# Kernel tuning notes

Hardware: AMD Instinct MI355X
Metric: run time of the kernel (lower is better)

Reference implementation:

```python
import jax, jax.numpy as jnp
import numpy as np

EPS = 1e-5

def conv1d(x, w, b, pad):
    # x: (B,Cin,T), w: (Cout,Cin,K)
    y = jax.lax.conv_general_dilated(x, w, (1,), [(pad, pad)],
                                     dimension_numbers=('NCW', 'OIW', 'NCW'))
    return y + b[None, :, None]

def group_norm(x, scale, bias, groups):
    B, C, T = x.shape
    xg = x.reshape(B, groups, C // groups, T)
    mu = xg.mean(axis=(2, 3), keepdims=True)
    var = xg.var(axis=(2, 3), keepdims=True)
    xn = ((xg - mu) * jax.lax.rsqrt(var + EPS)).reshape(B, C, T)
    return xn * scale[None, :, None] + bias[None, :, None]

def setup_inputs() -> dict:
    key = jax.random.key(0)
    ks = jax.random.split(key, 16)
    T, B = 1024, 128
    class_size, style_size, char_style_size = 80, 256, 64
    hidden, n_out = 128, 1
    cin = class_size + style_size + char_style_size  # 400
    def w(k, shape, fan_in):
        return jax.random.normal(k, shape, jnp.float32) * (1.0 / np.sqrt(fan_in))
    inp = {
        'input': jax.random.normal(ks[0], (T, B, class_size), jnp.float32),
        'g_style': jax.random.normal(ks[1], (B, style_size), jnp.float32),
        'spacing_style': jax.random.normal(ks[2], (B, 8), jnp.float32),
        'char_style': jax.random.normal(ks[3], (B, class_size, char_style_size), jnp.float32),
        'conv1_w': w(ks[4], (hidden, cin, 3), cin * 3),
        'conv1_b': jnp.zeros((hidden,), jnp.float32),
        'gn1_s': jnp.ones((hidden,), jnp.float32),
        'gn1_b': jnp.zeros((hidden,), jnp.float32),
        'conv2_w': w(ks[5], (hidden // 2, hidden, 3), hidden * 3),
        'conv2_b': jnp.zeros((hidden // 2,), jnp.float32),
        'gn2_s': jnp.ones((hidden // 2,), jnp.float32),
        'gn2_b': jnp.zeros((hidden // 2,), jnp.float32),
        'conv3_w': w(ks[6], (hidden // 4, hidden // 2, 3), (hidden // 2) * 3),
        'conv3_b': jnp.zeros((hidden // 4,), jnp.float32),
        'gn3_s': jnp.ones((hidden // 4,), jnp.float32),
        'gn3_b': jnp.zeros((hidden // 4,), jnp.float32),
        'conv4_w': w(ks[7], (n_out, hidden // 4, 1), hidden // 4),
        'conv4_b': jnp.zeros((n_out,), jnp.float32),
        'mean': jnp.full((1, n_out), 2.0, jnp.float32),
        'std': jnp.full((1, n_out), 1.0, jnp.float32),
    }
    return inp

def reference(input, g_style, spacing_style, char_style,
              conv1_w, conv1_b, gn1_s, gn1_b,
              conv2_w, conv2_b, gn2_s, gn2_b,
              conv3_w, conv3_b, gn3_s, gn3_b,
              conv4_w, conv4_b, mean, std):
    T, B, _ = input.shape
    # vectorized char-style gather (replaces the python double loop)
    text_chars = jnp.argmax(input, axis=2)                      # (T,B)
    input_style = char_style[jnp.arange(B)[None, :], text_chars]  # (T,B,Dc)
    gs = jnp.broadcast_to(g_style[None], (T,) + g_style.shape)    # (T,B,Ds)
    x = jnp.concatenate([input, gs, input_style], axis=2)         # (T,B,Cin)
    x = x.transpose(1, 2, 0)                                      # (B,Cin,T)
    x = jax.nn.relu(group_norm(conv1d(x, conv1_w, conv1_b, 1), gn1_s, gn1_b, 32))
    x = jax.nn.relu(group_norm(conv1d(x, conv2_w, conv2_b, 1), gn2_s, gn2_b, 32))
    x = jax.nn.relu(group_norm(conv1d(x, conv3_w, conv3_b, 1), gn3_s, gn3_b, 32))
    x = conv1d(x, conv4_w, conv4_b, 0)                            # (B,n_out,T)
    out = x.transpose(2, 0, 1)                                    # (T,B,n_out)
    return out * std + mean
```

## Files before the change

kernel.cpp:

```cpp
#include <hip/hip_runtime.h>
#include <hip/hip_bf16.h>

#define T_LEN 1024
#define BATCH 128
#define NM 131072

typedef __attribute__((ext_vector_type(8))) short short8;
typedef __attribute__((ext_vector_type(4))) float f32x4;
typedef __attribute__((ext_vector_type(4))) uint uint4e;

__device__ __forceinline__ float b2f(ushort u) {
  union { uint i; float f; } c; c.i = ((uint)u) << 16; return c.f;
}
__device__ __forceinline__ ushort f2b(float f) {
  __hip_bfloat16 h = __float2bfloat16(f);
  return *reinterpret_cast<ushort*>(&h);
}
__device__ __forceinline__ uint pack2(float a, float b) {
  return (uint)f2b(a) | ((uint)f2b(b) << 16);
}

__global__ __launch_bounds__(1024) void k_pre(const float* __restrict__ inp, const float* __restrict__ cs,
                                              ushort* __restrict__ X1) {
  __shared__ __align__(16) ushort L[8][32][160];
  int bid = blockIdx.x, tid = threadIdx.x;
  int b0 = (bid >> 5) * 8;
  int t0 = (bid & 31) * 32;
  int q = tid & 3;
  int u = tid >> 2;
  int bp = u & 7, tp = u >> 3;
  int b = b0 + bp, t = t0 + tp;
  int m = t*128 + b;
  const float* rp = inp + (size_t)m*80 + q*20;
  float v[20];
  #pragma unroll
  for (int i = 0; i < 5; ++i) {
    float4 u4 = *(const float4*)(rp + i*4);
    v[i*4+0]=u4.x; v[i*4+1]=u4.y; v[i*4+2]=u4.z; v[i*4+3]=u4.w;
  }
  float best = v[0]; int bi = q*20;
  #pragma unroll
  for (int i = 1; i < 20; ++i) if (v[i] > best) { best = v[i]; bi = q*20 + i; }
  #pragma unroll
  for (int d = 1; d <= 2; d <<= 1) {
    float ob = __shfl_xor(best, d);
    int   oi = __shfl_xor(bi, d);
    if (ob > best || (ob == best && oi < bi)) { best = ob; bi = oi; }
  }
  ushort* lr = &L[bp][tp][0];
  #pragma unroll
  for (int i = 0; i < 5; ++i) {
    uint2 pk; pk.x = pack2(v[i*4], v[i*4+1]); pk.y = pack2(v[i*4+2], v[i*4+3]);
    *(uint2*)(lr + q*20 + i*4) = pk;
  }
  *(uint2*)(lr + 80 + q*4) = make_uint2(0u, 0u);
  const float* crow = cs + ((size_t)b*80 + bi)*64 + q*16;
  #pragma unroll
  for (int i = 0; i < 4; ++i) {
    float4 u4 = *(const float4*)(crow + i*4);
    uint2 pk; pk.x = pack2(u4.x, u4.y); pk.y = pack2(u4.z, u4.w);
    *(uint2*)(lr + 96 + q*16 + i*4) = pk;
  }
  __syncthreads();
  int wave = tid >> 6, lane = tid & 63;
  int p = wave >> 1, h = wave & 1;
  ushort* dst = X1 + ((size_t)(b0 + p)*1024 + t0)*160 + h*2560;
  const ushort* src = &L[p][0][0] + h*2560;
  #pragma unroll
  for (int it = 0; it < 5; ++it) {
    int r = it*64 + lane;
    uint4e val = *(const uint4e*)(src + r*8);
    __builtin_nontemporal_store(val, (uint4e*)(dst + r*8));
  }
}

__global__ __launch_bounds__(256) void k_prep(const float* __restrict__ gsty,
    const float* __restrict__ w1, const float* __restrict__ b1,
    const float* __restrict__ w2, const float* __restrict__ w3,
    float* __restrict__ Gfull, float* __restrict__ Gk0, float* __restrict__ Gk2,
    ushort* __restrict__ Wp1, ushort* __restrict__ Wp2, ushort* __restrict__ Wp3) {
  int bid = blockIdx.x, tid = threadIdx.x;
  if (bid < 128) {
    int b = bid;
    __shared__ float gl[256];
    gl[tid] = gsty[b*256 + tid];
    __syncthreads();
    if (tid < 128) {
      int o = tid;
      const float* wr = w1 + (size_t)o*1200 + 240;
      float s0 = 0.f, s1 = 0.f, s2 = 0.f;
      for (int c = 0; c < 256; ++c) {
        float g = gl[c];
        s0 += wr[c*3+0]*g; s1 += wr[c*3+1]*g; s2 += wr[c*3+2]*g;
      }
      Gk0[b*128+o] = s0;
      Gk2[b*128+o] = s2;
      Gfull[b*128+o] = s0 + s1 + s2 + b1[o];
    }
  } else {
    int e = (bid - 128)*256 + tid;
    if (e < 61440) {
      int o = e / 480, r = e % 480, k = r / 160, c = r % 160;
      float v = 0.f;
      if (c < 80)       v = w1[(size_t)o*1200 + c*3 + k];
      else if (c >= 96) v = w1[(size_t)o*1200 + (336 + (c-96))*3 + k];
      Wp1[e] = f2b(v);
    } else if (e < 61440 + 24576) {
      int e2 = e - 61440;
      int o = e2/384, r = e2%384, k = r/128, c = r%128;
      Wp2[e2] = f2b(w2[(size_t)o*384 + c*3 + k]);
    } else if (e < 61440 + 24576 + 6144) {
      int e3 = e - 61440 - 24576;
      int o = e3/192, r = e3%192, k = r/64, c = r%64;
      Wp3[e3] = f2b(w3[(size_t)o*192 + c*3 + k]);
    }
  }
}

__device__ __forceinline__ uint4 c1_ldx(const ushort* X1b, int cc, int t0, int task) {
  int r = task >> 2, q = task & 3;
  int t = t0 - 1 + r;
  if (t >= 0 && t < T_LEN) return *(const uint4*)(X1b + (size_t)t*160 + cc*32 + q*8);
  return make_uint4(0u,0u,0u,0u);
}
__device__ __forceinline__ short8 c1_ldw(const ushort* Wp1, int cc, int task) {
  int o = task / 12, seg = task % 12;
  int k = seg >> 2, oct = seg & 3;
  return *(const short8*)(Wp1 + (size_t)o*480 + k*160 + cc*32 + oct*8);
}
__device__ __forceinline__ void c1_wrx(ushort (*Xsb)[40], int task, uint4 v) {
  int r = task >> 2, q = task & 3;
  *(uint4*)&Xsb[r][q*8] = v;
}
__device__ __forceinline__ void c1_wrw(ushort (*Wsb)[104], int task, short8 v) {
  int o = task / 12, seg = task % 12;
  *(short8*)&Wsb[o][seg*8] = v;
}

__global__ __launch_bounds__(256) void k_conv1(const ushort* __restrict__ X1, const ushort* __restrict__ Wp1,
    const float* __restrict__ Gfull, const float* __restrict__ Gk0, const float* __restrict__ Gk2,
    ushort* __restrict__ y1, float2* __restrict__ part1) {
  __shared__ __align__(16) ushort Xs[2][130][40];
  __shared__ __align__(16) ushort Ws[2][128][104];
  __shared__ float gf[128], g0v[128], g2v[128];
  __shared__ float ps[4][128], pq[4][128];
  int b = blockIdx.x, tt = blockIdx.y;
  int t0 = tt * 128;
  int tid = threadIdx.x, lane = tid & 63, wave = tid >> 6;
  int ln = lane & 15, lq = lane >> 4, wt = wave * 32;
  const ushort* X1b = X1 + (size_t)b * 163840;

  if (tid < 128) {
    gf[tid]  = Gfull[b*128 + tid];
    g0v[tid] = Gk0[b*128 + tid];
    g2v[tid] = Gk2[b*128 + tid];
  }
  f32x4 acc[2][8];
  #pragma unroll
  for (int m = 0; m < 2; ++m)
    #pragma unroll
    for (int n = 0; n < 8; ++n) { f32x4 z = {0.f,0.f,0.f,0.f}; acc[m][n] = z; }

  uint4 rx0, rx1, rx2;
  short8 rw[6];

  rx0 = c1_ldx(X1b, 0, t0, tid);
  rx1 = c1_ldx(X1b, 0, t0, tid + 256);
  if (tid < 8) rx2 = c1_ldx(X1b, 0, t0, tid + 512);
  #pragma unroll
  for (int i = 0; i < 6; ++i) rw[i] = c1_ldw(Wp1, 0, tid + i*256);
  c1_wrx(Xs[0], tid, rx0);
  c1_wrx(Xs[0], tid + 256, rx1);
  if (tid < 8) c1_wrx(Xs[0], tid + 512, rx2);
  #pragma unroll
  for (int i = 0; i < 6; ++i) c1_wrw(Ws[0], tid + i*256, rw[i]);
  __syncthreads();

  for (int cc = 0; cc < 5; ++cc) {
    bool more = (cc < 4);
    if (more) {
      rx0 = c1_ldx(X1b, cc+1, t0, tid);
      rx1 = c1_ldx(X1b, cc+1, t0, tid + 256);
      if (tid < 8) rx2 = c1_ldx(X1b, cc+1, t0, tid + 512);
      #pragma unroll
      for (int i = 0; i < 6; ++i) rw[i] = c1_ldw(Wp1, cc+1, tid + i*256);
    }
    int cur = cc & 1;
    #pragma unroll
    for (int k = 0; k < 3; ++k) {
      short8 a0 = *(const short8*)&Xs[cur][wt + ln + k][lq*8];
      short8 a1 = *(const short8*)&Xs[cur][wt + 16 + ln + k][lq*8];
      #pragma unroll
      for (int nt = 0; nt < 8; ++nt) {
        short8 bb = *(const short8*)&Ws[cur][nt*16 + ln][k*32 + lq*8];
        acc[0][nt] = __builtin_amdgcn_mfma_f32_16x16x32_bf16(a0, bb, acc[0][nt], 0, 0, 0);
        acc[1][nt] = __builtin_amdgcn_mfma_f32_16x16x32_bf16(a1, bb, acc[1][nt], 0, 0, 0);
      }
    }
    if (more) {
      int nxt = cur ^ 1;
      c1_wrx(Xs[nxt], tid, rx0);
      c1_wrx(Xs[nxt], tid + 256, rx1);
      if (tid < 8) c1_wrx(Xs[nxt], tid + 512, rx2);
      #pragma unroll
      for (int i = 0; i < 6; ++i) c1_wrw(Ws[nxt], tid + i*256, rw[i]);
    }
    __syncthreads();
  }

  #pragma unroll
  for (int nt = 0; nt < 8; ++nt) {
    int o = nt*16 + ln;
    float add = gf[o];
    float s = 0.f, sq = 0.f;
    #pragma unroll
    for (int mt = 0; mt < 2; ++mt) {
      int tb = t0 + wt + mt*16 + lq*4;
      float vv[4];
      #pragma unroll
      for (int r = 0; r < 4; ++r) {
        float v = acc[mt][nt][r] + add;
        int t = tb + r;
        if (t == 0) v -= g0v[o];
        if (t == T_LEN-1) v -= g2v[o];
        vv[r] = v; s += v; sq += v*v;
      }
      uint2 pk;
      pk.x = pack2(vv[0], vv[1]);
      pk.y = pack2(vv[2], vv[3]);
      *(uint2*)(y1 + ((size_t)b*128 + o)*T_LEN + tb) = pk;
    }
    s  += __shfl_xor(s, 16);  s  += __shfl_xor(s, 32);
    sq += __shfl_xor(sq, 16); sq += __shfl_xor(sq, 32);
    if (lane < 16) { ps[wave][o] = s; pq[wave][o] = sq; }
  }
  __syncthreads();
  if (tid < 128) {
    float S = ps[0][tid]+ps[1][tid]+ps[2][tid]+ps[3][tid];
    float Q = pq[0][tid]+pq[1][tid]+pq[2][tid]+pq[3][tid];
    part1[((size_t)b*128 + tid)*8 + tt] = make_float2(S, Q);
  }
}

__device__ __forceinline__ short8 mid_ldw(const ushort* Wp, int cin, int cc, int task) {
  int o = task / 12, seg = task % 12;
  int k = seg >> 2, oct = seg & 3;
  return *(const short8*)(Wp + ((size_t)o*3 + k)*cin + cc*32 + oct*8);
}
__device__ __forceinline__ void mid_wrw(ushort (*Wsb)[104], int task, short8 v) {
  int o = task / 12, seg = task % 12;
  *(short8*)&Wsb[o][seg*8] = v;
}

template<int NC, int CO, int NT, int CPG>
__global__ __launch_bounds__(256) void k_convmid(const ushort* __restrict__ xin,
    const ushort* __restrict__ Wp, const float* __restrict__ bias,
    const float2* __restrict__ partin, const float* __restrict__ gs, const float* __restrict__ gb,
    ushort* __restrict__ yout, float2* __restrict__ part) {
  constexpr int CIN = NC*32;
  constexpr int NG = CIN/CPG;
  __shared__ __align__(16) ushort Xs[2][130][40];
  __shared__ __align__(16) ushort Ws[2][CO][104];
  __shared__ float2 affl[CIN];
  __shared__ float ssb[CIN], qqb[CIN];
  __shared__ float2 gmr[NG];
  __shared__ float bl[CO];
  __shared__ float ps[4][CO], pq[4][CO];
  int b = blockIdx.x, tt = blockIdx.y, t0 = tt*128;
  int tid = threadIdx.x, lane = tid & 63, wave = tid >> 6;
  int ln = lane & 15, lq = lane >> 4, wt = wave*32;
  int cp = (tid & 15)*2, j = tid >> 4;
  int er = (tid < 32) ? 0 : 129, eci = tid & 31;
  const ushort* xb = xin + (size_t)b * CIN * T_LEN;

  if (tid < CIN) {
    const float2* p = partin + (size_t)(b*CIN + tid)*8;
    float S = 0.f, Q = 0.f;
    #pragma unroll
    for (int j2 = 0; j2 < 8; ++j2) { float2 v = p[j2]; S += v.x; Q += v.y; }
    ssb[tid] = S; qqb[tid] = Q;
  }
  if (tid < CO)  bl[tid]  = bias[tid];

  f32x4 acc[2][NT];
  #pragma unroll
  for (int m = 0; m < 2; ++m)
    #pragma unroll
    for (int n = 0; n < NT; ++n) { f32x4 z = {0.f,0.f,0.f,0.f}; acc[m][n] = z; }

  short8 v0, v1;
  ushort ev = 0;
  short8 rw0, rw1, rw2;
  int te = t0 - 1 + er;

  {
    const ushort* s0 = xb + (size_t)cp * T_LEN + t0 + j*8;
    v0 = *(const short8*)s0;
    v1 = *(const short8*)(s0 + T_LEN);
    ev = 0;
    if (tid < 64 && te >= 0 && te < T_LEN) ev = xb[(size_t)eci * T_LEN + te];
    rw0 = mid_ldw(Wp, CIN, 0, tid);
    if constexpr (CO == 64) {
      rw1 = mid_ldw(Wp, CIN, 0, tid + 256);
      rw2 = mid_ldw(Wp, CIN, 0, tid + 512);
    } else {
      if (tid < 128) rw1 = mid_ldw(Wp, CIN, 0, tid + 256);
    }
  }
  __syncthreads();
  if (tid < NG) {
    float S = 0.f, Q = 0.f;
    #pragma unroll
    for (int ci = 0; ci < CPG; ++ci) { S += ssb[tid*CPG+ci]; Q += qqb[tid*CPG+ci]; }
    float invn = 1.f / (float)(CPG * T_LEN);
    float m = S * invn;
    float var = Q * invn - m*m;
    gmr[tid] = make_float2(m, rsqrtf(var + 1e-5f));
  }
  __syncthreads();
  if (tid < CIN) {
    float2 mr = gmr[tid / CPG];
    float a = mr.y * gs[tid];
    affl[tid] = make_float2(a, gb[tid] - mr.x * a);
  }
  __syncthreads();
  {
    float2 A0 = affl[cp], A1 = affl[cp+1];
    #pragma unroll
    for (int e = 0; e < 8; ++e) {
      float f0 = fmaxf(0.f, b2f((ushort)v0[e])*A0.x + A0.y);
      float f1 = fmaxf(0.f, b2f((ushort)v1[e])*A1.x + A1.y);
      *(uint*)&Xs[0][1 + j*8 + e][cp] = pack2(f0, f1);
    }
    if (tid < 64) {
      ushort val = 0;
      if (te >= 0 && te < T_LEN) { float2 A = affl[eci]; val = f2b(fmaxf(0.f, b2f(ev)*A.x + A.y)); }
      Xs[0][er][eci] = val;
    }
    mid_wrw(Ws[0], tid, rw0);
    if constexpr (CO == 64) {
      mid_wrw(Ws[0], tid + 256, rw1);
      mid_wrw(Ws[0], tid + 512, rw2);
    } else {
      if (tid < 128) mid_wrw(Ws[0], tid + 256, rw1);
    }
  }
  __syncthreads();

  for (int cc = 0; cc < NC; ++cc) {
    bool more = (cc + 1 < NC);
    if (more) {
      const ushort* s0 = xb + (size_t)((cc+1)*32 + cp) * T_LEN + t0 + j*8;
      v0 = *(const short8*)s0;
      v1 = *(const short8*)(s0 + T_LEN);
      ev = 0;
      if (tid < 64 && te >= 0 && te < T_LEN) ev = xb[(size_t)((cc+1)*32 + eci) * T_LEN + te];
      rw0 = mid_ldw(Wp, CIN, cc+1, tid);
      if constexpr (CO == 64) {
        rw1 = mid_ldw(Wp, CIN, cc+1, tid + 256);
        rw2 = mid_ldw(Wp, CIN, cc+1, tid + 512);
      } else {
        if (tid < 128) rw1 = mid_ldw(Wp, CIN, cc+1, tid + 256);
      }
    }
    int cur = cc & 1;
    #pragma unroll
    for (int k = 0; k < 3; ++k) {
      short8 a0 = *(const short8*)&Xs[cur][wt + ln + k][lq*8];
      short8 a1 = *(const short8*)&Xs[cur][wt + 16 + ln + k][lq*8];
      #pragma unroll
      for (int nt = 0; nt < NT; ++nt) {
        short8 bb = *(const short8*)&Ws[cur][nt*16 + ln][k*32 + lq*8];
        acc[0][nt] = __builtin_amdgcn_mfma_f32_16x16x32_bf16(a0, bb, acc[0][nt], 0, 0, 0);
        acc[1][nt] = __builtin_amdgcn_mfma_f32_16x16x32_bf16(a1, bb, acc[1][nt], 0, 0, 0);
      }
    }
    if (more) {
      int nxt = cur ^ 1;
      float2 A0 = affl[(cc+1)*32 + cp], A1 = affl[(cc+1)*32 + cp + 1];
      #pragma unroll
      for (int e = 0; e < 8; ++e) {
        float f0 = fmaxf(0.f, b2f((ushort)v0[e])*A0.x + A0.y);
        float f1 = fmaxf(0.f, b2f((ushort)v1[e])*A1.x + A1.y);
        *(uint*)&Xs[nxt][1 + j*8 + e][cp] = pack2(f0, f1);
      }
      if (tid < 64) {
        ushort val = 0;
        if (te >= 0 && te < T_LEN) { float2 A = affl[(cc+1)*32 + eci]; val = f2b(fmaxf(0.f, b2f(ev)*A.x + A.y)); }
        Xs[nxt][er][eci] = val;
      }
      mid_wrw(Ws[nxt], tid, rw0);
      if constexpr (CO == 64) {
        mid_wrw(Ws[nxt], tid + 256, rw1);
        mid_wrw(Ws[nxt], tid + 512, rw2);
      } else {
        if (tid < 128) mid_wrw(Ws[nxt], tid + 256, rw1);
      }
    }
    __syncthreads();
  }

  #pragma unroll
  for (int nt = 0; nt < NT; ++nt) {
    int o = nt*16 + ln;
    float add = bl[o];
    float s = 0.f, sq = 0.f;
    #pragma unroll
    for (int mt = 0; mt < 2; ++mt) {
      int tb = t0 + wt + mt*16 + lq*4;
      float vv[4];
      #pragma unroll
      for (int r = 0; r < 4; ++r) {
        float v = acc[mt][nt][r] + add;
        vv[r] = v; s += v; sq += v*v;
      }
      uint2 pk;
      pk.x = pack2(vv[0], vv[1]);
      pk.y = pack2(vv[2], vv[3]);
      *(uint2*)(yout + ((size_t)b*CO + o)*T_LEN + tb) = pk;
    }
    s  += __shfl_xor(s, 16);  s  += __shfl_xor(s, 32);
    sq += __shfl_xor(sq, 16); sq += __shfl_xor(sq, 32);
    if (lane < 16) { ps[wave][o] = s; pq[wave][o] = sq; }
  }
  __syncthreads();
  if (tid < CO) {
    float S = ps[0][tid]+ps[1][tid]+ps[2][tid]+ps[3][tid];
    float Q = pq[0][tid]+pq[1][tid]+pq[2][tid]+pq[3][tid];
    part[((size_t)b*CO + tid)*8 + tt] = make_float2(S, Q);
  }
}

__global__ __launch_bounds__(256) void k_final(const ushort* __restrict__ y3, const float2* __restrict__ part3,
    const float* __restrict__ s3, const float* __restrict__ b3,
    const float* __restrict__ w4, const float* __restrict__ b4,
    const float* __restrict__ mn, const float* __restrict__ sd, float* __restrict__ out) {
  int b = blockIdx.x;
  int t = blockIdx.y * 256 + threadIdx.x;
  __shared__ float wl[32];
  __shared__ float2 al[32];
  if (threadIdx.x < 32) {
    int c = threadIdx.x;
    const float2* p = part3 + (size_t)(b*32 + c)*8;
    float S = 0.f, Q = 0.f;
    #pragma unroll
    for (int j = 0; j < 8; ++j) { float2 v = p[j]; S += v.x; Q += v.y; }
    float invn = 1.f / (float)T_LEN;
    float m = S * invn;
    float var = Q * invn - m*m;
    float rs = rsqrtf(var + 1e-5f);
    float a = rs * s3[c];
    al[c] = make_float2(a, b3[c] - m*a);
    wl[c] = w4[c];
  }
  __syncthreads();
  float s = b4[0];
  #pragma unroll 8
  for (int c = 0; c < 32; ++c) {
    float v = b2f(y3[((size_t)b*32 + c)*T_LEN + t]);
    float2 A = al[c];
    s += wl[c] * fmaxf(0.f, v*A.x + A.y);
  }
  out[(size_t)t*BATCH + b] = s*sd[0] + mn[0];
}

extern "C" void kernel_launch(void* const* d_in, const int* in_sizes, int n_in,
                              void* d_out, int out_size, void* d_ws, size_t ws_size,
                              hipStream_t stream) {
  const float* inp  = (const float*)d_in[0];
  const float* gsty = (const float*)d_in[1];
  const float* cs   = (const float*)d_in[3];
  const float* w1   = (const float*)d_in[4];
  const float* b1   = (const float*)d_in[5];
  const float* gn1s = (const float*)d_in[6];
  const float* gn1b = (const float*)d_in[7];
  const float* w2   = (const float*)d_in[8];
  const float* b2   = (const float*)d_in[9];
  const float* gn2s = (const float*)d_in[10];
  const float* gn2b = (const float*)d_in[11];
  const float* w3   = (const float*)d_in[12];
  const float* b3   = (const float*)d_in[13];
  const float* gn3s = (const float*)d_in[14];
  const float* gn3b = (const float*)d_in[15];
  const float* w4   = (const float*)d_in[16];
  const float* b4   = (const float*)d_in[17];
  const float* mn   = (const float*)d_in[18];
  const float* sd   = (const float*)d_in[19];
  float* out = (float*)d_out;
  ushort* wsu = (ushort*)d_ws;

  ushort* X1  = wsu;
  ushort* Wp1 = X1 + (size_t)20971520;
  ushort* Wp2 = Wp1 + 61440;
  ushort* Wp3 = Wp2 + 24576;
  float* Gfull = (float*)(Wp3 + 6144);
  float* Gk0   = Gfull + 16384;
  float* Gk2   = Gk0 + 16384;
  ushort* y1 = (ushort*)(Gk2 + 16384);
  ushort* y2 = y1 + (size_t)NM*128;
  ushort* y3 = y2 + (size_t)NM*64;
  float2* part1 = (float2*)(y3 + (size_t)NM*32);
  float2* part2 = part1 + 131072;
  float2* part3 = part2 + 65536;

  k_pre<<<512, 1024, 0, stream>>>(inp, cs, X1);
  k_prep<<<488, 256, 0, stream>>>(gsty, w1, b1, w2, w3,
                                  Gfull, Gk0, Gk2, Wp1, Wp2, Wp3);
  k_conv1<<<dim3(128,8), 256, 0, stream>>>(X1, Wp1, Gfull, Gk0, Gk2, y1, part1);
  k_convmid<4,64,4,4><<<dim3(128,8), 256, 0, stream>>>(y1, Wp2, b2, part1, gn1s, gn1b, y2, part2);
  k_convmid<2,32,2,2><<<dim3(128,8), 256, 0, stream>>>(y2, Wp3, b3, part2, gn2s, gn2b, y3, part3);
  k_final<<<dim3(128,4), 256, 0, stream>>>(y3, part3, gn3s, gn3b, w4, b4, mn, sd, out);
}
```

Before: 101.7 us.

## Gather char-style rows inside conv1 instead of materializing padded input tensor

The preprocessing kernel now writes only the bf16 one-hot input in its native (T,B,80) layout plus an argmax index per position, rather than a transposed, padded 160-channel tensor that also holds the gathered char-style rows. Conv1 reads the class channels directly from that layout and gathers the char-style rows from the fp32 source table using the indices staged in shared memory, converting to bf16 on the fly. This cuts the intermediate write and read traffic roughly in half. The cost is strided per-row loads in conv1 (80-element rows spaced by batch) and scattered fp32 gathers, which may coalesce less well.

```diff
diff --git a/kernel.cpp b/kernel.cpp
--- a/kernel.cpp
+++ b/kernel.cpp
@@ -7,7 +7,6 @@
 
 typedef __attribute__((ext_vector_type(8))) short short8;
 typedef __attribute__((ext_vector_type(4))) float f32x4;
-typedef __attribute__((ext_vector_type(4))) uint uint4e;
 
 __device__ __forceinline__ float b2f(ushort u) {
   union { uint i; float f; } c; c.i = ((uint)u) << 16; return c.f;
@@ -20,18 +19,12 @@
   return (uint)f2b(a) | ((uint)f2b(b) << 16);
 }
 
-__global__ __launch_bounds__(1024) void k_pre(const float* __restrict__ inp, const float* __restrict__ cs,
-                                              ushort* __restrict__ X1) {
-  __shared__ __align__(16) ushort L[8][32][160];
-  int bid = blockIdx.x, tid = threadIdx.x;
-  int b0 = (bid >> 5) * 8;
-  int t0 = (bid & 31) * 32;
+__global__ __launch_bounds__(256) void k_pre(const float* __restrict__ inp,
+                                             ushort* __restrict__ Xm, int* __restrict__ idx) {
+  int tid = threadIdx.x;
+  int m = blockIdx.x * 64 + (tid >> 2);
   int q = tid & 3;
-  int u = tid >> 2;
-  int bp = u & 7, tp = u >> 3;
-  int b = b0 + bp, t = t0 + tp;
-  int m = t*128 + b;
-  const float* rp = inp + (size_t)m*80 + q*20;
+  const float* rp = inp + (size_t)m * 80 + q * 20;
   float v[20];
   #pragma unroll
   for (int i = 0; i < 5; ++i) {
@@ -47,30 +40,12 @@
     int   oi = __shfl_xor(bi, d);
     if (ob > best || (ob == best && oi < bi)) { best = ob; bi = oi; }
   }
-  ushort* lr = &L[bp][tp][0];
+  if (q == 0) idx[m] = bi;
+  ushort* orow = Xm + (size_t)m * 80 + q * 20;
   #pragma unroll
   for (int i = 0; i < 5; ++i) {
     uint2 pk; pk.x = pack2(v[i*4], v[i*4+1]); pk.y = pack2(v[i*4+2], v[i*4+3]);
-    *(uint2*)(lr + q*20 + i*4) = pk;
-  }
-  *(uint2*)(lr + 80 + q*4) = make_uint2(0u, 0u);
-  const float* crow = cs + ((size_t)b*80 + bi)*64 + q*16;
-  #pragma unroll
-  for (int i = 0; i < 4; ++i) {
-    float4 u4 = *(const float4*)(crow + i*4);
-    uint2 pk; pk.x = pack2(u4.x, u4.y); pk.y = pack2(u4.z, u4.w);
-    *(uint2*)(lr + 96 + q*16 + i*4) = pk;
-  }
-  __syncthreads();
-  int wave = tid >> 6, lane = tid & 63;
-  int p = wave >> 1, h = wave & 1;
-  ushort* dst = X1 + ((size_t)(b0 + p)*1024 + t0)*160 + h*2560;
-  const ushort* src = &L[p][0][0] + h*2560;
-  #pragma unroll
-  for (int it = 0; it < 5; ++it) {
-    int r = it*64 + lane;
-    uint4e val = *(const uint4e*)(src + r*8);
-    __builtin_nontemporal_store(val, (uint4e*)(dst + r*8));
+    *(uint2*)(orow + i*4) = pk;
   }
 }
 
@@ -117,10 +92,31 @@
   }
 }
 
-__device__ __forceinline__ uint4 c1_ldx(const ushort* X1b, int cc, int t0, int task) {
+__device__ __forceinline__ uint4 c1_ldx16(const ushort* __restrict__ Xm, int b, int cc, int t0, int task) {
   int r = task >> 2, q = task & 3;
   int t = t0 - 1 + r;
-  if (t >= 0 && t < T_LEN) return *(const uint4*)(X1b + (size_t)t*160 + cc*32 + q*8);
+  int c8 = cc*32 + q*8;
+  if (t >= 0 && t < T_LEN && c8 < 80)
+    return *(const uint4*)(Xm + ((size_t)t*BATCH + b)*80 + c8);
+  return make_uint4(0u,0u,0u,0u);
+}
+__device__ __forceinline__ uint4 packf(float4 a, float4 b) {
+  uint4 p;
+  p.x = pack2(a.x, a.y); p.y = pack2(a.z, a.w);
+  p.z = pack2(b.x, b.y); p.w = pack2(b.z, b.w);
+  return p;
+}
+__device__ __forceinline__ uint4 c1_ldcs(const float* __restrict__ cs, const int* idxs,
+                                         int b, int cc, int t0, int task) {
+  int r = task >> 2, q = task & 3;
+  int t = t0 - 1 + r;
+  if (t >= 0 && t < T_LEN) {
+    int jc = idxs[r];
+    const float* src = cs + ((size_t)b*80 + jc)*64 + (cc-3)*32 + q*8;
+    float4 fa = *(const float4*)src;
+    float4 fb = *(const float4*)(src + 4);
+    return packf(fa, fb);
+  }
   return make_uint4(0u,0u,0u,0u);
 }
 __device__ __forceinline__ short8 c1_ldw(const ushort* Wp1, int cc, int task) {
@@ -137,19 +133,24 @@
   *(short8*)&Wsb[o][seg*8] = v;
 }
 
-__global__ __launch_bounds__(256) void k_conv1(const ushort* __restrict__ X1, const ushort* __restrict__ Wp1,
+__global__ __launch_bounds__(256) void k_conv1(const ushort* __restrict__ Xm, const float* __restrict__ cs,
+    const int* __restrict__ idx, const ushort* __restrict__ Wp1,
     const float* __restrict__ Gfull, const float* __restrict__ Gk0, const float* __restrict__ Gk2,
     ushort* __restrict__ y1, float2* __restrict__ part1) {
   __shared__ __align__(16) ushort Xs[2][130][40];
   __shared__ __align__(16) ushort Ws[2][128][104];
   __shared__ float gf[128], g0v[128], g2v[128];
   __shared__ float ps[4][128], pq[4][128];
+  __shared__ int idxs[130];
   int b = blockIdx.x, tt = blockIdx.y;
   int t0 = tt * 128;
   int tid = threadIdx.x, lane = tid & 63, wave = tid >> 6;
   int ln = lane & 15, lq = lane >> 4, wt = wave * 32;
-  const ushort* X1b = X1 + (size_t)b * 163840;
-
+
+  if (tid < 130) {
+    int t = t0 - 1 + tid;
+    idxs[tid] = (t >= 0 && t < T_LEN) ? idx[t*BATCH + b] : 0;
+  }
   if (tid < 128) {
     gf[tid]  = Gfull[b*128 + tid];
     g0v[tid] = Gk0[b*128 + tid];
@@ -164,9 +165,9 @@
   uint4 rx0, rx1, rx2;
   short8 rw[6];
 
-  rx0 = c1_ldx(X1b, 0, t0, tid);
-  rx1 = c1_ldx(X1b, 0, t0, tid + 256);
-  if (tid < 8) rx2 = c1_ldx(X1b, 0, t0, tid + 512);
+  rx0 = c1_ldx16(Xm, b, 0, t0, tid);
+  rx1 = c1_ldx16(Xm, b, 0, t0, tid + 256);
+  if (tid < 8) rx2 = c1_ldx16(Xm, b, 0, t0, tid + 512);
   #pragma unroll
   for (int i = 0; i < 6; ++i) rw[i] = c1_ldw(Wp1, 0, tid + i*256);
   c1_wrx(Xs[0], tid, rx0);
@@ -179,9 +180,15 @@
   for (int cc = 0; cc < 5; ++cc) {
     bool more = (cc < 4);
     if (more) {
-      rx0 = c1_ldx(X1b, cc+1, t0, tid);
-      rx1 = c1_ldx(X1b, cc+1, t0, tid + 256);
-      if (tid < 8) rx2 = c1_ldx(X1b, cc+1, t0, tid + 512);
+      if (cc + 1 < 3) {
+        rx0 = c1_ldx16(Xm, b, cc+1, t0, tid);
+        rx1 = c1_ldx16(Xm, b, cc+1, t0, tid + 256);
+        if (tid < 8) rx2 = c1_ldx16(Xm, b, cc+1, t0, tid + 512);
+      } else {
+        rx0 = c1_ldcs(cs, idxs, b, cc+1, t0, tid);
+        rx1 = c1_ldcs(cs, idxs, b, cc+1, t0, tid + 256);
+        if (tid < 8) rx2 = c1_ldcs(cs, idxs, b, cc+1, t0, tid + 512);
+      }
       #pragma unroll
       for (int i = 0; i < 6; ++i) rw[i] = c1_ldw(Wp1, cc+1, tid + i*256);
     }
@@ -489,8 +496,9 @@
   float* out = (float*)d_out;
   ushort* wsu = (ushort*)d_ws;
 
-  ushort* X1  = wsu;
-  ushort* Wp1 = X1 + (size_t)20971520;
+  ushort* Xm  = wsu;
+  int*    idx = (int*)(Xm + (size_t)10485760);
+  ushort* Wp1 = (ushort*)(idx + NM);
   ushort* Wp2 = Wp1 + 61440;
   ushort* Wp3 = Wp2 + 24576;
   float* Gfull = (float*)(Wp3 + 6144);
@@ -503,10 +511,10 @@
   float2* part2 = part1 + 131072;
   float2* part3 = part2 + 65536;
 
-  k_pre<<<512, 1024, 0, stream>>>(inp, cs, X1);
+  k_pre<<<2048, 256, 0, stream>>>(inp, Xm, idx);
   k_prep<<<488, 256, 0, stream>>>(gsty, w1, b1, w2, w3,
                                   Gfull, Gk0, Gk2, Wp1, Wp2, Wp3);
-  k_conv1<<<dim3(128,8), 256, 0, stream>>>(X1, Wp1, Gfull, Gk0, Gk2, y1, part1);
+  k_conv1<<<dim3(128,8), 256, 0, stream>>>(Xm, cs, idx, Wp1, Gfull, Gk0, Gk2, y1, part1);
   k_convmid<4,64,4,4><<<dim3(128,8), 256, 0, stream>>>(y1, Wp2, b2, part1, gn1s, gn1b, y2, part2);
   k_convmid<2,32,2,2><<<dim3(128,8), 256, 0, stream>>>(y2, Wp3, b3, part2, gn2s, gn2b, y3, part3);
   k_final<<<dim3(128,4), 256, 0, stream>>>(y3, part3, gn3s, gn3b, w4, b4, mn, sd, out);
```

After: 98.50 us. 1.03x faster.
